# Optimization experiments

Measured on AMD Instinct MI355X. Metric: run time of the kernel, lower is better.

Reference implementation:

```python
import jax, jax.numpy as jnp
import numpy as np

B, S, H_IN, H = 32, 1024, 1024, 1024


def setup_inputs() -> dict:
    key = jax.random.key(0)
    k1, k2, k3, k4, k5, k6, k7 = jax.random.split(key, 7)
    hidden = jax.random.normal(k1, (B, H), dtype=jnp.float32)
    encoder_outputs = jax.random.normal(k2, (S, B, H_IN), dtype=jnp.float32)
    mask = jax.random.randint(k3, (B, S), 0, 2).astype(bool)
    mask = mask.at[:, 0].set(False)  # ensure at least one unmasked position per row
    lim1 = 1.0 / np.sqrt(H_IN + H)
    lim2 = 1.0 / np.sqrt(H)
    W1 = jax.random.uniform(k4, (H, H_IN + H), minval=-lim1, maxval=lim1, dtype=jnp.float32)
    b1 = jax.random.uniform(k5, (H,), minval=-lim1, maxval=lim1, dtype=jnp.float32)
    W2 = jax.random.uniform(k6, (1, H), minval=-lim2, maxval=lim2, dtype=jnp.float32)
    b2 = jax.random.uniform(k7, (1,), minval=-lim2, maxval=lim2, dtype=jnp.float32)
    return {"hidden": hidden, "encoder_outputs": encoder_outputs, "mask": mask,
            "W1": W1, "b1": b1, "W2": W2, "b2": b2}


def reference(hidden, encoder_outputs, mask, W1, b1, W2, b2):
    # encoder_outputs: [S,B,Hin] -> [B,S,Hin]; hidden: [B,H] broadcast over S.
    enc = jnp.transpose(encoder_outputs, (1, 0, 2))  # [B,S,Hin]
    # cat([enc, hidden], -1) @ W1.T == enc @ W1_enc.T + hidden @ W1_hid.T (avoids materializing concat)
    W1_enc, W1_hid = W1[:, :enc.shape[-1]], W1[:, enc.shape[-1]:]
    a1 = jnp.einsum('bsi,hi->bsh', enc, W1_enc) + (hidden @ W1_hid.T)[:, None, :] + b1
    a1 = jnp.tanh(a1)                                # [B,S,H]
    scores = jnp.einsum('bsh,h->bs', a1, W2[0]) + b2[0]  # [B,S]
    scores = jnp.where(mask, -jnp.inf, scores)
    attn = jax.nn.softmax(scores, axis=-1)           # softmax over seq dim
    return attn[:, None, :]                          # [B,1,S]
```

## Files before the change

kernel.cpp:

```cpp
#include <hip/hip_runtime.h>
#include <hip/hip_bf16.h>
#include <cstdint>


#define BM 128
#define BN 128
#define BK 64
#define NKT 16

typedef short  s16x8 __attribute__((ext_vector_type(8)));
typedef float  f32x4 __attribute__((ext_vector_type(4)));
typedef unsigned int u32;
typedef unsigned short u16;
typedef unsigned long long u64;

__device__ static inline u32 f2bf(float f) {
    u32 u = __float_as_uint(f);
    return (u + 0x7fffu + ((u >> 16) & 1u)) >> 16;
}
__device__ static inline u32 pk2(float a, float b) {
    return f2bf(a) | (f2bf(b) << 16);
}

__device__ static inline void gload_lds16(const void* g, void* l) {
    __builtin_amdgcn_global_load_lds(
        (const __attribute__((address_space(1))) u32*)g,
        (__attribute__((address_space(3))) u32*)l, 16, 0, 0);
}

__global__ __launch_bounds__(256) void prep_k(const float* __restrict__ W1,
                                              const float* __restrict__ hidden,
                                              const float* __restrict__ b1,
                                              const void*  __restrict__ maskv,
                                              u16*   __restrict__ Wb,
                                              float* __restrict__ hv,
                                              int*   __restrict__ sidx,
                                              int*   __restrict__ cnt,
                                              float* __restrict__ scores) {
    const int bx = blockIdx.x, t = threadIdx.x;
    const int wid = t >> 6, lane = t & 63;
    __shared__ int sflag[4];

    if (bx < 512) {
        const int i = bx * 256 + t;
        const int n = i >> 7, gc = i & 127;
        const float4 v0 = *(const float4*)(W1 + (size_t)n * 2048 + gc * 8);
        const float4 v1 = *(const float4*)(W1 + (size_t)n * 2048 + gc * 8 + 4);
        uint4 o; o.x = pk2(v0.x, v0.y); o.y = pk2(v0.z, v0.w);
        o.z = pk2(v1.x, v1.y); o.w = pk2(v1.z, v1.w);
        *(uint4*)(Wb + (size_t)n * 1024 + gc * 8) = o;
    } else if (bx < 768) {
        const int h = (bx - 512) * 4 + wid;
        const float4* wrow = (const float4*)(W1 + (size_t)h * 2048 + 1024);
        float4 w[4];
#pragma unroll
        for (int q = 0; q < 4; q++) w[q] = wrow[lane + 64 * q];
        for (int b = 0; b < 32; b++) {
            const float4* hb = (const float4*)(hidden + (size_t)b * 1024);
            float p = 0.f;
#pragma unroll
            for (int q = 0; q < 4; q++) {
                float4 x = hb[lane + 64 * q];
                p = fmaf(w[q].x, x.x, fmaf(w[q].y, x.y, fmaf(w[q].z, x.z, fmaf(w[q].w, x.w, p))));
            }
#pragma unroll
            for (int off = 1; off < 64; off <<= 1) p += __shfl_xor(p, off);
            if (lane == 0) hv[(size_t)b * 1024 + h] = p + b1[h];
        }
    } else if (bx < 776) {
        const u32* mw = (const u32*)maskv;
        int f = 0;
#pragma unroll
        for (int j = 0; j < 32; j++) f |= (mw[t * 32 + j] > 1u) ? 1 : 0;
        const int anyf = __any(f);
        if (lane == 0) sflag[wid] = anyf;
        __syncthreads();
        const int bytemode = sflag[0] | sflag[1] | sflag[2] | sflag[3];

        const int b = (bx - 768) * 4 + wid;
        int base = 0;
        for (int c = 0; c < 16; c++) {
            const int s = c * 64 + lane;
            int m;
            if (bytemode) m = ((const unsigned char*)maskv)[(size_t)b * 1024 + s];
            else          m = ((const int*)maskv)[(size_t)b * 1024 + s];
            const u64 bal = __ballot(m == 0);
            if (m == 0) {
                const int off = (int)__popcll(bal & ((1ull << lane) - 1ull));
                sidx[(size_t)b * 1024 + base + off] = s;
            }
            base += (int)__popcll(bal);
        }
        if (lane == 0) cnt[b] = base;
        for (int j = base + lane; j < 1024; j += 64) sidx[(size_t)b * 1024 + j] = 0;
    } else {
        const int i = (bx - 776) * 256 + t;
        ((float4*)scores)[i] = make_float4(0.f, 0.f, 0.f, 0.f);
    }
}

__global__ __launch_bounds__(256) void conv_k(const float* __restrict__ enc,
                                              const int* __restrict__ sidx,
                                              const int* __restrict__ cnt,
                                              u16* __restrict__ encC) {
    const int bid = blockIdx.x, t = threadIdx.x;
    const int xcd = bid & 7, w = bid >> 3;
    const int b = xcd * 4 + (w >> 8);
    const int j0 = (w & 255) * 4;
    const int c = cnt[b];
    if (j0 >= ((c + 127) & ~127)) return;
#pragma unroll
    for (int r = 0; r < 4; r++) {
        const int j = j0 + r;
        const int s = (j < c) ? sidx[(size_t)b * 1024 + j] : 0;
        const float4 v = ((const float4*)(enc + ((size_t)s * 32 + b) * 1024))[t];
        uint2 o; o.x = pk2(v.x, v.y); o.y = pk2(v.z, v.w);
        *(uint2*)(encC + ((size_t)b * 1024 + j) * 1024 + t * 4) = o;
    }
}

__global__ __launch_bounds__(256, 4) void gemm_c(
    const u16* __restrict__ encC,
    const u16* __restrict__ Wb,
    const int* __restrict__ sidx,
    const int* __restrict__ cnt,
    const float* __restrict__ hv,
    const float* __restrict__ W2,
    float*      __restrict__ scores)
{
    __shared__ u16 As[BM * BK];
    __shared__ u16 Bs[BN * BK];

    const int tid = threadIdx.x;
    const int bid = blockIdx.x;
    const int xcd = bid & 7, slot = bid >> 3;
    const int mstrip = xcd * 32 + (slot >> 3);
    const int nt = slot & 7;
    const int b = mstrip >> 3, mtile = mstrip & 7;
    const int c = cnt[b];
    if (mtile * 128 >= c) return;

    const int srow = tid >> 3, sc16 = tid & 7;
    const u16* asrc = encC + ((size_t)b * 1024 + mtile * 128 + srow) * 1024 + sc16 * 8;
    const u16* bsrc = Wb + ((size_t)(nt * BN) + srow) * 1024 + sc16 * 8;

    const int wid = tid >> 6, lane = tid & 63;
    const int wr = wid >> 1, wc = wid & 1;
    const int lhi = lane >> 4, llo = lane & 15;

    f32x4 acc[4][4] = {};

    for (int kt = 0; kt < NKT; kt++) {
        const size_t ko = (size_t)kt * 64;
#pragma unroll
        for (int j = 0; j < 4; j++)
            gload_lds16(asrc + ko + (size_t)j * 32 * 1024, &As[(j * 256 + tid) * 8]);
#pragma unroll
        for (int j = 0; j < 4; j++)
            gload_lds16(bsrc + ko + (size_t)j * 32 * 1024, &Bs[(j * 256 + tid) * 8]);
        __syncthreads();
#pragma unroll
        for (int kk = 0; kk < 2; kk++) {
            s16x8 af[4], bfr[4];
#pragma unroll
            for (int f = 0; f < 4; f++)
                af[f] = *(const s16x8*)&As[(wr * 64 + f * 16 + llo) * BK + kk * 32 + lhi * 8];
#pragma unroll
            for (int f = 0; f < 4; f++)
                bfr[f] = *(const s16x8*)&Bs[(wc * 64 + f * 16 + llo) * BK + kk * 32 + lhi * 8];
#pragma unroll
            for (int fi = 0; fi < 4; fi++)
#pragma unroll
                for (int fj = 0; fj < 4; fj++)
                    acc[fi][fj] = __builtin_amdgcn_mfma_f32_16x16x32_bf16(af[fi], bfr[fj], acc[fi][fj], 0, 0, 0);
        }
        __syncthreads();
    }

    const float* hvb = hv + (size_t)b * 1024;
    float hvv[4], w2v[4];
#pragma unroll
    for (int fj = 0; fj < 4; fj++) {
        const int n = nt * BN + wc * 64 + fj * 16 + llo;
        hvv[fj] = hvb[n];
        w2v[fj] = W2[n];
    }
#pragma unroll
    for (int fi = 0; fi < 4; fi++) {
#pragma unroll
        for (int r = 0; r < 4; r++) {
            float sum = 0.f;
#pragma unroll
            for (int fj = 0; fj < 4; fj++) {
                const float x = acc[fi][fj][r] + hvv[fj];
                const float e = __expf(2.f * x);
                const float t = 1.f - 2.f / (e + 1.f);
                sum = fmaf(t, w2v[fj], sum);
            }
            sum += __shfl_xor(sum, 1);
            sum += __shfl_xor(sum, 2);
            sum += __shfl_xor(sum, 4);
            sum += __shfl_xor(sum, 8);
            if (llo == 0) {
                const int j = mtile * 128 + wr * 64 + fi * 16 + lhi * 4 + r;
                if (j < c) {
                    const int s = sidx[(size_t)b * 1024 + j];
                    atomicAdd(&scores[(size_t)b * 1024 + s], sum);
                }
            }
        }
    }
}

__global__ __launch_bounds__(256) void softmax_k(const float* __restrict__ scores,
                                                 const void* __restrict__ maskv,
                                                 float* __restrict__ out) {
    const int b = blockIdx.x, t = threadIdx.x;
    const int wid = t >> 6, lane = t & 63;
    const u32* mw = (const u32*)maskv;
    int f = 0;
#pragma unroll
    for (int j = 0; j < 32; j++) f |= (mw[t * 32 + j] > 1u) ? 1 : 0;
    __shared__ int sflag[4];
    const int anyf = __any(f);
    if (lane == 0) sflag[wid] = anyf;
    __syncthreads();
    const int bytemode = sflag[0] | sflag[1] | sflag[2] | sflag[3];

    int m0, m1, m2, m3;
    if (bytemode) {
        const uchar4 mk = ((const uchar4*)((const unsigned char*)maskv + (size_t)b * 1024))[t];
        m0 = mk.x; m1 = mk.y; m2 = mk.z; m3 = mk.w;
    } else {
        const int4 mk = ((const int4*)((const int*)maskv + (size_t)b * 1024))[t];
        m0 = mk.x; m1 = mk.y; m2 = mk.z; m3 = mk.w;
    }
    const float4 sc = ((const float4*)(scores + (size_t)b * 1024))[t];
    const float v0 = m0 ? -1e30f : sc.x;
    const float v1 = m1 ? -1e30f : sc.y;
    const float v2 = m2 ? -1e30f : sc.z;
    const float v3 = m3 ? -1e30f : sc.w;
    float mx = fmaxf(fmaxf(v0, v1), fmaxf(v2, v3));
#pragma unroll
    for (int off = 1; off < 64; off <<= 1) mx = fmaxf(mx, __shfl_xor(mx, off));
    __shared__ float redm[4], reds[4];
    if (lane == 0) redm[wid] = mx;
    __syncthreads();
    mx = fmaxf(fmaxf(redm[0], redm[1]), fmaxf(redm[2], redm[3]));
    const float e0 = m0 ? 0.f : __expf(v0 - mx);
    const float e1 = m1 ? 0.f : __expf(v1 - mx);
    const float e2 = m2 ? 0.f : __expf(v2 - mx);
    const float e3 = m3 ? 0.f : __expf(v3 - mx);
    float s = e0 + e1 + e2 + e3;
#pragma unroll
    for (int off = 1; off < 64; off <<= 1) s += __shfl_xor(s, off);
    if (lane == 0) reds[wid] = s;
    __syncthreads();
    s = reds[0] + reds[1] + reds[2] + reds[3];
    const float inv = 1.f / s;
    float4 o; o.x = e0 * inv; o.y = e1 * inv; o.z = e2 * inv; o.w = e3 * inv;
    ((float4*)(out + (size_t)b * 1024))[t] = o;
}

extern "C" void kernel_launch(void* const* d_in, const int* in_sizes, int n_in,
                              void* d_out, int out_size, void* d_ws, size_t ws_size,
                              hipStream_t stream) {
    const float* hidden = (const float*)d_in[0];
    const float* enc    = (const float*)d_in[1];
    const void*  mask   = d_in[2];
    const float* W1 = (const float*)d_in[3];
    const float* b1 = (const float*)d_in[4];
    const float* W2 = (const float*)d_in[5];
    float* out = (float*)d_out;

    char* ws = (char*)d_ws;
    float* ws_scores = (float*)ws;
    float* ws_hv     = (float*)(ws + (128u << 10));
    u16*   ws_Wb     = (u16*)(ws + (256u << 10));
    int*   ws_cnt    = (int*)(ws + (2304u << 10));
    int*   ws_sidx   = (int*)(ws + (2432u << 10));
    u16*   ws_encC   = (u16*)(ws + (4096u << 10));

    prep_k<<<808, 256, 0, stream>>>(W1, hidden, b1, mask, ws_Wb, ws_hv, ws_sidx, ws_cnt, ws_scores);
    conv_k<<<8192, 256, 0, stream>>>(enc, ws_sidx, ws_cnt, ws_encC);
    gemm_c<<<2048, 256, 0, stream>>>(ws_encC, ws_Wb, ws_sidx, ws_cnt, ws_hv, W2, ws_scores);
    softmax_k<<<32, 256, 0, stream>>>(ws_scores, mask, out);
}
```

Measured before the change: 115.2 us.

## Rewrite gemm as 256x256-tile, 4-stage pipelined LDS kernel with swizzle

```diff
diff --git a/kernel.cpp b/kernel.cpp
--- a/kernel.cpp
+++ b/kernel.cpp
@@ -3,10 +3,7 @@
 #include <cstdint>
 
 
-#define BM 128
-#define BN 128
-#define BK 64
-#define NKT 16
+#define NKT32 32
 
 typedef short  s16x8 __attribute__((ext_vector_type(8)));
 typedef float  f32x4 __attribute__((ext_vector_type(4)));
@@ -108,7 +105,7 @@
     const int b = xcd * 4 + (w >> 8);
     const int j0 = (w & 255) * 4;
     const int c = cnt[b];
-    if (j0 >= ((c + 127) & ~127)) return;
+    if (j0 >= ((c + 255) & ~255)) return;
 #pragma unroll
     for (int r = 0; r < 4; r++) {
         const int j = j0 + r;
@@ -119,7 +116,7 @@
     }
 }
 
-__global__ __launch_bounds__(256, 4) void gemm_c(
+__global__ __launch_bounds__(512, 2) void gemm_r4(
     const u16* __restrict__ encC,
     const u16* __restrict__ Wb,
     const int* __restrict__ sidx,
@@ -128,65 +125,102 @@
     const float* __restrict__ W2,
     float*      __restrict__ scores)
 {
-    __shared__ u16 As[BM * BK];
-    __shared__ u16 Bs[BN * BK];
+    __shared__ u16 lds[4 * 16384];
 
     const int tid = threadIdx.x;
     const int bid = blockIdx.x;
-    const int xcd = bid & 7, slot = bid >> 3;
-    const int mstrip = xcd * 32 + (slot >> 3);
-    const int nt = slot & 7;
-    const int b = mstrip >> 3, mtile = mstrip & 7;
+    const int xcd = bid & 7, idx = bid >> 3;
+    const int strip = xcd * 16 + (idx >> 2);
+    const int nt = idx & 3;
+    const int b = strip >> 2, mt = strip & 3;
     const int c = cnt[b];
-    if (mtile * 128 >= c) return;
-
-    const int srow = tid >> 3, sc16 = tid & 7;
-    const u16* asrc = encC + ((size_t)b * 1024 + mtile * 128 + srow) * 1024 + sc16 * 8;
-    const u16* bsrc = Wb + ((size_t)(nt * BN) + srow) * 1024 + sc16 * 8;
+    if (mt * 256 >= c) return;
+
+    const u16* abase = encC + ((size_t)b * 1024 + mt * 256) * 1024;
+    const u16* bbase = Wb + (size_t)(nt * 256) * 1024;
 
     const int wid = tid >> 6, lane = tid & 63;
-    const int wr = wid >> 1, wc = wid & 1;
+    const int wm = wid >> 2, wn = wid & 3;
     const int lhi = lane >> 4, llo = lane & 15;
 
-    f32x4 acc[4][4] = {};
-
-    for (int kt = 0; kt < NKT; kt++) {
-        const size_t ko = (size_t)kt * 64;
-#pragma unroll
-        for (int j = 0; j < 4; j++)
-            gload_lds16(asrc + ko + (size_t)j * 32 * 1024, &As[(j * 256 + tid) * 8]);
-#pragma unroll
-        for (int j = 0; j < 4; j++)
-            gload_lds16(bsrc + ko + (size_t)j * 32 * 1024, &Bs[(j * 256 + tid) * 8]);
-        __syncthreads();
-#pragma unroll
-        for (int kk = 0; kk < 2; kk++) {
-            s16x8 af[4], bfr[4];
-#pragma unroll
-            for (int f = 0; f < 4; f++)
-                af[f] = *(const s16x8*)&As[(wr * 64 + f * 16 + llo) * BK + kk * 32 + lhi * 8];
-#pragma unroll
-            for (int f = 0; f < 4; f++)
-                bfr[f] = *(const s16x8*)&Bs[(wc * 64 + f * 16 + llo) * BK + kk * 32 + lhi * 8];
-#pragma unroll
-            for (int fi = 0; fi < 4; fi++)
-#pragma unroll
-                for (int fj = 0; fj < 4; fj++)
-                    acc[fi][fj] = __builtin_amdgcn_mfma_f32_16x16x32_bf16(af[fi], bfr[fj], acc[fi][fj], 0, 0, 0);
-        }
-        __syncthreads();
-    }
+    f32x4 acc[8][4] = {};
+
+#define STAGE(KT)                                                                \
+    {                                                                            \
+        u16* Asl = &lds[((KT) & 3) * 16384];                                     \
+        u16* Bsl = Asl + 8192;                                                   \
+        const size_t ko = (size_t)(KT) * 32;                                     \
+        _Pragma("unroll")                                                        \
+        for (int j = 0; j < 2; j++) {                                            \
+            const int cix = j * 512 + tid;                                       \
+            const int row = cix >> 2, cp = cix & 3;                              \
+            const int lc = cp ^ (row & 3);                                       \
+            gload_lds16(abase + (size_t)row * 1024 + ko + lc * 8, Asl + cix * 8);\
+            gload_lds16(bbase + (size_t)row * 1024 + ko + lc * 8, Bsl + cix * 8);\
+        }                                                                        \
+    }
+
+#define COMPUTE(KT)                                                              \
+    {                                                                            \
+        const u16* Asl = &lds[((KT) & 3) * 16384];                               \
+        const u16* Bsl = Asl + 8192;                                             \
+        s16x8 bf[4], af[8];                                                      \
+        _Pragma("unroll")                                                        \
+        for (int fj = 0; fj < 4; fj++) {                                         \
+            const int row = wn * 64 + fj * 16 + llo;                             \
+            const int cp = lhi ^ (row & 3);                                      \
+            bf[fj] = *(const s16x8*)&Bsl[row * 32 + cp * 8];                     \
+        }                                                                        \
+        _Pragma("unroll")                                                        \
+        for (int fi = 0; fi < 8; fi++) {                                         \
+            const int row = wm * 128 + fi * 16 + llo;                            \
+            const int cp = lhi ^ (row & 3);                                      \
+            af[fi] = *(const s16x8*)&Asl[row * 32 + cp * 8];                     \
+        }                                                                        \
+        __builtin_amdgcn_s_setprio(1);                                           \
+        _Pragma("unroll")                                                        \
+        for (int fi = 0; fi < 8; fi++)                                           \
+            _Pragma("unroll")                                                    \
+            for (int fj = 0; fj < 4; fj++)                                       \
+                acc[fi][fj] = __builtin_amdgcn_mfma_f32_16x16x32_bf16(           \
+                    af[fi], bf[fj], acc[fi][fj], 0, 0, 0);                       \
+        __builtin_amdgcn_s_setprio(0);                                           \
+    }
+
+    STAGE(0); STAGE(1); STAGE(2);
+
+    for (int kt = 0; kt < 28; kt++) {
+        asm volatile("s_waitcnt vmcnt(8)" ::: "memory");
+        __builtin_amdgcn_s_barrier();
+        STAGE(kt + 3);
+        COMPUTE(kt);
+    }
+    asm volatile("s_waitcnt vmcnt(8)" ::: "memory");
+    __builtin_amdgcn_s_barrier();
+    STAGE(31);
+    COMPUTE(28);
+    asm volatile("s_waitcnt vmcnt(8)" ::: "memory");
+    __builtin_amdgcn_s_barrier();
+    COMPUTE(29);
+    asm volatile("s_waitcnt vmcnt(4)" ::: "memory");
+    __builtin_amdgcn_s_barrier();
+    COMPUTE(30);
+    asm volatile("s_waitcnt vmcnt(0)" ::: "memory");
+    __builtin_amdgcn_s_barrier();
+    COMPUTE(31);
+#undef STAGE
+#undef COMPUTE
 
     const float* hvb = hv + (size_t)b * 1024;
     float hvv[4], w2v[4];
 #pragma unroll
     for (int fj = 0; fj < 4; fj++) {
-        const int n = nt * BN + wc * 64 + fj * 16 + llo;
+        const int n = nt * 256 + wn * 64 + fj * 16 + llo;
         hvv[fj] = hvb[n];
         w2v[fj] = W2[n];
     }
 #pragma unroll
-    for (int fi = 0; fi < 4; fi++) {
+    for (int fi = 0; fi < 8; fi++) {
 #pragma unroll
         for (int r = 0; r < 4; r++) {
             float sum = 0.f;
@@ -202,7 +236,7 @@
             sum += __shfl_xor(sum, 4);
             sum += __shfl_xor(sum, 8);
             if (llo == 0) {
-                const int j = mtile * 128 + wr * 64 + fi * 16 + lhi * 4 + r;
+                const int j = mt * 256 + wm * 128 + fi * 16 + lhi * 4 + r;
                 if (j < c) {
                     const int s = sidx[(size_t)b * 1024 + j];
                     atomicAdd(&scores[(size_t)b * 1024 + s], sum);
@@ -283,6 +317,6 @@
 
     prep_k<<<808, 256, 0, stream>>>(W1, hidden, b1, mask, ws_Wb, ws_hv, ws_sidx, ws_cnt, ws_scores);
     conv_k<<<8192, 256, 0, stream>>>(enc, ws_sidx, ws_cnt, ws_encC);
-    gemm_c<<<2048, 256, 0, stream>>>(ws_encC, ws_Wb, ws_sidx, ws_cnt, ws_hv, W2, ws_scores);
+    gemm_r4<<<512, 512, 0, stream>>>(ws_encC, ws_Wb, ws_sidx, ws_cnt, ws_hv, W2, ws_scores);
     softmax_k<<<32, 256, 0, stream>>>(ws_scores, mask, out);
 }
```

Measured after the change: 135.6 us. +17.7%, slower.
